# Kernel optimization log

Hardware: AMD Instinct MI355X
Metric: run time of the kernel (lower is better)

Reference implementation:

```python
import jax, jax.numpy as jnp
import numpy as np

NEG = jnp.float32(-9e15)
SLOPE = 0.2  # LeakyReLU negative slope used in LocalAggregator


def setup_inputs() -> dict:
    key = jax.random.key(0)
    k1, k2, k3, k4, k5, k6, k7 = jax.random.split(key, 7)
    B, N, D, V = 32, 200, 100, 50000
    stdv = 1.0 / np.sqrt(D)
    inputs = jax.random.randint(k1, (B, N), 0, V)
    adj = jax.random.randint(k2, (B, N, N), 0, 5).astype(jnp.int32)
    mask_item = jnp.ones((B, N), dtype=jnp.int32)
    emb = jax.random.uniform(k3, (V, D), jnp.float32, -stdv, stdv)
    a0 = jax.random.uniform(k4, (D, 1), jnp.float32, -stdv, stdv)
    a1 = jax.random.uniform(k5, (D, 1), jnp.float32, -stdv, stdv)
    a2 = jax.random.uniform(k6, (D, 1), jnp.float32, -stdv, stdv)
    a3 = jax.random.uniform(k7, (D, 1), jnp.float32, -stdv, stdv)
    return {"inputs": inputs, "adj": adj, "mask_item": mask_item,
            "emb": emb, "a0": a0, "a1": a1, "a2": a2, "a3": a3}


def reference(inputs, adj, mask_item, emb, a0, a1, a2, a3):
    # h: [B, N, D] session item embeddings
    h = emb[inputs]
    # e_k[b,i,j] = leaky_relu(sum_d h[b,i,d]*h[b,j,d]*a_k[d])
    # (equivalent to the original (h_i * h_j) @ a_k without the BxNxNxD blowup)
    def edge_score(a):
        s = jnp.einsum('bid,bjd->bij', h * a[:, 0][None, None, :], h)
        return jax.nn.leaky_relu(s, SLOPE)
    e0, e1, e2, e3 = edge_score(a0), edge_score(a1), edge_score(a2), edge_score(a3)
    alpha = jnp.where(adj == 1, e0, NEG)
    alpha = jnp.where(adj == 2, e1, alpha)
    alpha = jnp.where(adj == 3, e2, alpha)
    alpha = jnp.where(adj == 4, e3, alpha)
    alpha = jax.nn.softmax(alpha, axis=-1)  # [B, N, N]
    # weighted aggregation over neighbors; dropout_local is inactive in eval
    return jnp.einsum('bij,bjd->bid', alpha, h)
```

## Files before the change

kernel.cpp:

```cpp
#include <hip/hip_runtime.h>
#include <math.h>

#define NEGV  (-9e15f)
#define SLOPE 0.2f

typedef __fp16 f16;
typedef __fp16 f16x4 __attribute__((ext_vector_type(4)));
typedef __fp16 f16x8 __attribute__((ext_vector_type(8)));
typedef float  f32x4 __attribute__((ext_vector_type(4)));

__global__ __launch_bounds__(256) void gat_mfma_kernel(
    const int*   __restrict__ inputs,
    const int*   __restrict__ adj,
    const float* __restrict__ emb,
    const float* __restrict__ a0, const float* __restrict__ a1,
    const float* __restrict__ a2, const float* __restrict__ a3,
    float*       __restrict__ out)
{
    const int b   = blockIdx.x / 13;
    const int i0  = (blockIdx.x % 13) * 16;
    const int tid = threadIdx.x;

    __shared__ f16 HF[200][112];
    __shared__ __align__(16) unsigned char ubuf[4 * 16 * 96 * 2];
    __shared__ f16 GT[4][16][32];
    __shared__ int   sidx[200];
    __shared__ float redmax[16][4];
    __shared__ float redsum[16][4];

    f16 (*GF)[16][96] = (f16(*)[16][96])ubuf;
    f16 (*ST)[24]     = (f16(*)[24])ubuf;

    for (int t = tid; t < 200; t += 256) sidx[t] = inputs[b * 200 + t];
    __syncthreads();

    if (tid < 200) {
        const float4* src = (const float4*)(emb + (size_t)sidx[tid] * 100);
        f16x4* dst = (f16x4*)&HF[tid][0];
        #pragma unroll
        for (int c = 0; c < 25; ++c) {
            const float4 v = src[c];
            f16x4 o; o[0] = (f16)v.x; o[1] = (f16)v.y; o[2] = (f16)v.z; o[3] = (f16)v.w;
            dst[c] = o;
        }
        const f16x4 z = {(f16)0.f, (f16)0.f, (f16)0.f, (f16)0.f};
        dst[25] = z; dst[26] = z; dst[27] = z;
    }

    for (int t = tid; t < 4 * 16 * 24; t += 256) {
        const int kk = t / (16 * 24);
        const int rm = t % (16 * 24);
        const int il = rm / 24;
        const int c  = rm % 24;
        const float* ak = (kk == 0) ? a0 : (kk == 1) ? a1 : (kk == 2) ? a2 : a3;
        const int gi = i0 + il;
        f16x4 o = {(f16)0.f, (f16)0.f, (f16)0.f, (f16)0.f};
        if (gi < 200) {
            const float4 hv = ((const float4*)(emb + (size_t)sidx[gi] * 100))[c];
            const float4 av = ((const float4*)ak)[c];
            o[0] = (f16)(hv.x * av.x); o[1] = (f16)(hv.y * av.y);
            o[2] = (f16)(hv.z * av.z); o[3] = (f16)(hv.w * av.w);
        }
        ((f16x4*)&GF[kk][il][0])[c] = o;
    }

    for (int t = tid; t < 4 * 16 * 8; t += 256) {
        const int kk = t / (16 * 8);
        const int rm = t % (16 * 8);
        const int il = rm / 8;
        const int c  = rm % 8;
        f16x4 o = {(f16)0.f, (f16)0.f, (f16)0.f, (f16)0.f};
        const int gi = i0 + il;
        if (c == 4 && gi < 200) {
            const float* ak = (kk == 0) ? a0 : (kk == 1) ? a1 : (kk == 2) ? a2 : a3;
            const float* hi = emb + (size_t)sidx[gi] * 100;
            o[0] = (f16)(hi[96] * ak[96]); o[1] = (f16)(hi[97] * ak[97]);
            o[2] = (f16)(hi[98] * ak[98]); o[3] = (f16)(hi[99] * ak[99]);
        }
        ((f16x4*)&GT[kk][il][0])[c] = o;
    }
    __syncthreads();

    const int wave = tid >> 6;
    const int lane = tid & 63;
    const int lj   = lane & 15;
    const int quad = lane >> 4;
    const int rbase = quad * 4;

    f32x4 acc[4][4];
    #pragma unroll
    for (int kk = 0; kk < 4; ++kk)
        #pragma unroll
        for (int jt = 0; jt < 4; ++jt)
            acc[kk][jt] = (f32x4){0.f, 0.f, 0.f, 0.f};

    #pragma unroll
    for (int jtidx = 0; jtidx < 4; ++jtidx) {
        const int j  = (wave + 4 * jtidx) * 16 + lj;
        const int jr = (j < 200) ? j : 0;
        const f16x8* Brow = (const f16x8*)&HF[jr][0];
        const f16x8 b0 = Brow[quad];
        const f16x8 b1 = Brow[4 + quad];
        const f16x8 b2 = Brow[8 + quad];
        const f16x8 b3 = Brow[10 + quad];
        #pragma unroll
        for (int kk = 0; kk < 4; ++kk) {
            const f16x8* Arow = (const f16x8*)&GF[kk][lj][0];
            f32x4 c = acc[kk][jtidx];
            c = __builtin_amdgcn_mfma_f32_16x16x32_f16(Arow[quad],     b0, c, 0, 0, 0);
            c = __builtin_amdgcn_mfma_f32_16x16x32_f16(Arow[4 + quad], b1, c, 0, 0, 0);
            c = __builtin_amdgcn_mfma_f32_16x16x32_f16(Arow[8 + quad], b2, c, 0, 0, 0);
            c = __builtin_amdgcn_mfma_f32_16x16x32_f16(((const f16x8*)&GT[kk][lj][0])[quad], b3, c, 0, 0, 0);
            acc[kk][jtidx] = c;
        }
    }

    float sel[4][4];
    #pragma unroll
    for (int jtidx = 0; jtidx < 4; ++jtidx) {
        const int j = (wave + 4 * jtidx) * 16 + lj;
        #pragma unroll
        for (int reg = 0; reg < 4; ++reg) {
            const int gi = i0 + rbase + reg;
            float s = NEGV;
            if (j < 200 && gi < 200) {
                const int k = adj[(size_t)(b * 200 + gi) * 200 + j];
                if (k >= 1 && k <= 4) {
                    const float v = (k == 1) ? acc[0][jtidx][reg]
                                  : (k == 2) ? acc[1][jtidx][reg]
                                  : (k == 3) ? acc[2][jtidx][reg]
                                  :            acc[3][jtidx][reg];
                    s = (v >= 0.f) ? v : SLOPE * v;
                }
            }
            sel[jtidx][reg] = s;
        }
    }

    #pragma unroll
    for (int reg = 0; reg < 4; ++reg) {
        float m = fmaxf(fmaxf(sel[0][reg], sel[1][reg]), fmaxf(sel[2][reg], sel[3][reg]));
        #pragma unroll
        for (int off = 1; off <= 8; off <<= 1) m = fmaxf(m, __shfl_xor(m, off, 16));
        if (lj == 0) redmax[rbase + reg][wave] = m;
    }
    __syncthreads();
    float m4[4], lsum[4];
    #pragma unroll
    for (int reg = 0; reg < 4; ++reg) {
        const float* rr = redmax[rbase + reg];
        m4[reg] = fmaxf(fmaxf(rr[0], rr[1]), fmaxf(rr[2], rr[3]));
        lsum[reg] = 0.f;
    }
    float e[4][4];
    #pragma unroll
    for (int jtidx = 0; jtidx < 4; ++jtidx)
        #pragma unroll
        for (int reg = 0; reg < 4; ++reg) {
            e[jtidx][reg] = __expf(sel[jtidx][reg] - m4[reg]);
            lsum[reg] += e[jtidx][reg];
        }
    #pragma unroll
    for (int reg = 0; reg < 4; ++reg) {
        float s = lsum[reg];
        #pragma unroll
        for (int off = 1; off <= 8; off <<= 1) s += __shfl_xor(s, off, 16);
        if (lj == 0) redsum[rbase + reg][wave] = s;
    }
    __syncthreads();
    float inv[4];
    #pragma unroll
    for (int reg = 0; reg < 4; ++reg) {
        const float* rr = redsum[rbase + reg];
        inv[reg] = 1.0f / (rr[0] + rr[1] + rr[2] + rr[3]);
    }
    #pragma unroll
    for (int jtidx = 0; jtidx < 4; ++jtidx) {
        const int j = (wave + 4 * jtidx) * 16 + lj;
        if (j < 200) {
            #pragma unroll
            for (int reg = 0; reg < 4; ++reg)
                ST[j][rbase + reg] = (f16)(e[jtidx][reg] * inv[reg]);
        }
    }
    __syncthreads();

    const int ig = tid & 7;
    const int dq = tid >> 3;
    f32x4 o[16];
    #pragma unroll
    for (int i = 0; i < 16; ++i) o[i] = (f32x4){0.f, 0.f, 0.f, 0.f};
    if (dq < 25) {
        for (int jj = 0; jj < 25; ++jj) {
            const int j = ig * 25 + jj;
            const f16x8 w0 = *(const f16x8*)&ST[j][0];
            const f16x8 w1 = *(const f16x8*)&ST[j][8];
            const f16x4 hv = *(const f16x4*)&HF[j][dq * 4];
            const float h0 = (float)hv[0], h1 = (float)hv[1],
                        h2 = (float)hv[2], h3 = (float)hv[3];
            #pragma unroll
            for (int i = 0; i < 8; ++i) {
                const float w = (float)w0[i];
                o[i][0] += w * h0; o[i][1] += w * h1; o[i][2] += w * h2; o[i][3] += w * h3;
            }
            #pragma unroll
            for (int i = 0; i < 8; ++i) {
                const float w = (float)w1[i];
                o[8 + i][0] += w * h0; o[8 + i][1] += w * h1; o[8 + i][2] += w * h2; o[8 + i][3] += w * h3;
            }
        }
    }
    #pragma unroll
    for (int i = 0; i < 16; ++i)
        #pragma unroll
        for (int c = 0; c < 4; ++c)
            #pragma unroll
            for (int off = 1; off <= 4; off <<= 1)
                o[i][c] += __shfl_xor(o[i][c], off, 8);
    if (ig == 0 && dq < 25) {
        #pragma unroll
        for (int i = 0; i < 16; ++i) {
            const int gi = i0 + i;
            if (gi < 200)
                ((f32x4*)out)[(size_t)(b * 200 + gi) * 25 + dq] = o[i];
        }
    }
}

extern "C" void kernel_launch(void* const* d_in, const int* in_sizes, int n_in,
                              void* d_out, int out_size, void* d_ws, size_t ws_size,
                              hipStream_t stream) {
    const int*   inputs = (const int*)  d_in[0];
    const int*   adj    = (const int*)  d_in[1];
    const float* emb    = (const float*)d_in[3];
    const float* a0     = (const float*)d_in[4];
    const float* a1     = (const float*)d_in[5];
    const float* a2     = (const float*)d_in[6];
    const float* a3     = (const float*)d_in[7];
    float*       out    = (float*)d_out;

    gat_mfma_kernel<<<dim3(32 * 13), dim3(256), 0, stream>>>(inputs, adj, emb, a0, a1, a2, a3, out);
}
```

Before: 106.1 us.

## Drop shared-memory HF staging; read neighbor embeddings directly from global memory

Removes the per-block fp16 copy of all 200 session embeddings into LDS. The MFMA B operands and the aggregation loop now read embeddings straight from global memory, converting to fp16 only where needed. The aggregation step keeps weights and embeddings in fp32. The A-operand staging is merged into one padded 128-wide buffer, removing the separate tail buffer. This trades LDS footprint and fill time for more global/L2 traffic, with repeated scattered gathers of the same rows across the 13 blocks per batch.

```diff
diff --git a/kernel.cpp b/kernel.cpp
--- a/kernel.cpp
+++ b/kernel.cpp
@@ -9,7 +9,7 @@
 typedef __fp16 f16x8 __attribute__((ext_vector_type(8)));
 typedef float  f32x4 __attribute__((ext_vector_type(4)));
 
-__global__ __launch_bounds__(256) void gat_mfma_kernel(
+__global__ __launch_bounds__(256) void gat_v9_kernel(
     const int*   __restrict__ inputs,
     const int*   __restrict__ adj,
     const float* __restrict__ emb,
@@ -21,70 +21,38 @@
     const int i0  = (blockIdx.x % 13) * 16;
     const int tid = threadIdx.x;
 
-    __shared__ f16 HF[200][112];
-    __shared__ __align__(16) unsigned char ubuf[4 * 16 * 96 * 2];
-    __shared__ f16 GT[4][16][32];
+    __shared__ f16   GF[4][16][136];
+    __shared__ float ST[200][20];
     __shared__ int   sidx[200];
-    __shared__ float redmax[16][4];
-    __shared__ float redsum[16][4];
-
-    f16 (*GF)[16][96] = (f16(*)[16][96])ubuf;
-    f16 (*ST)[24]     = (f16(*)[24])ubuf;
+    __shared__ float redm[16][4];
+    __shared__ float reds[16][4];
 
     for (int t = tid; t < 200; t += 256) sidx[t] = inputs[b * 200 + t];
     __syncthreads();
 
-    if (tid < 200) {
-        const float4* src = (const float4*)(emb + (size_t)sidx[tid] * 100);
-        f16x4* dst = (f16x4*)&HF[tid][0];
-        #pragma unroll
-        for (int c = 0; c < 25; ++c) {
-            const float4 v = src[c];
-            f16x4 o; o[0] = (f16)v.x; o[1] = (f16)v.y; o[2] = (f16)v.z; o[3] = (f16)v.w;
-            dst[c] = o;
-        }
-        const f16x4 z = {(f16)0.f, (f16)0.f, (f16)0.f, (f16)0.f};
-        dst[25] = z; dst[26] = z; dst[27] = z;
-    }
-
-    for (int t = tid; t < 4 * 16 * 24; t += 256) {
-        const int kk = t / (16 * 24);
-        const int rm = t % (16 * 24);
-        const int il = rm / 24;
-        const int c  = rm % 24;
-        const float* ak = (kk == 0) ? a0 : (kk == 1) ? a1 : (kk == 2) ? a2 : a3;
+    const float* aks[4] = {a0, a1, a2, a3};
+
+    for (int t = tid; t < 4 * 16 * 34; t += 256) {
+        const int kk = t / (16 * 34);
+        const int rm = t % (16 * 34);
+        const int il = rm / 34;
+        const int c  = rm % 34;
         const int gi = i0 + il;
         f16x4 o = {(f16)0.f, (f16)0.f, (f16)0.f, (f16)0.f};
-        if (gi < 200) {
+        if (gi < 200 && c < 25) {
             const float4 hv = ((const float4*)(emb + (size_t)sidx[gi] * 100))[c];
-            const float4 av = ((const float4*)ak)[c];
+            const float4 av = ((const float4*)aks[kk])[c];
             o[0] = (f16)(hv.x * av.x); o[1] = (f16)(hv.y * av.y);
             o[2] = (f16)(hv.z * av.z); o[3] = (f16)(hv.w * av.w);
         }
         ((f16x4*)&GF[kk][il][0])[c] = o;
     }
-
-    for (int t = tid; t < 4 * 16 * 8; t += 256) {
-        const int kk = t / (16 * 8);
-        const int rm = t % (16 * 8);
-        const int il = rm / 8;
-        const int c  = rm % 8;
-        f16x4 o = {(f16)0.f, (f16)0.f, (f16)0.f, (f16)0.f};
-        const int gi = i0 + il;
-        if (c == 4 && gi < 200) {
-            const float* ak = (kk == 0) ? a0 : (kk == 1) ? a1 : (kk == 2) ? a2 : a3;
-            const float* hi = emb + (size_t)sidx[gi] * 100;
-            o[0] = (f16)(hi[96] * ak[96]); o[1] = (f16)(hi[97] * ak[97]);
-            o[2] = (f16)(hi[98] * ak[98]); o[3] = (f16)(hi[99] * ak[99]);
-        }
-        ((f16x4*)&GT[kk][il][0])[c] = o;
-    }
-    __syncthreads();
-
-    const int wave = tid >> 6;
-    const int lane = tid & 63;
-    const int lj   = lane & 15;
-    const int quad = lane >> 4;
+    __syncthreads();
+
+    const int wave  = tid >> 6;
+    const int lane  = tid & 63;
+    const int lj    = lane & 15;
+    const int quad  = lane >> 4;
     const int rbase = quad * 4;
 
     f32x4 acc[4][4];
@@ -95,30 +63,43 @@
             acc[kk][jt] = (f32x4){0.f, 0.f, 0.f, 0.f};
 
     #pragma unroll
-    for (int jtidx = 0; jtidx < 4; ++jtidx) {
-        const int j  = (wave + 4 * jtidx) * 16 + lj;
-        const int jr = (j < 200) ? j : 0;
-        const f16x8* Brow = (const f16x8*)&HF[jr][0];
-        const f16x8 b0 = Brow[quad];
-        const f16x8 b1 = Brow[4 + quad];
-        const f16x8 b2 = Brow[8 + quad];
-        const f16x8 b3 = Brow[10 + quad];
+    for (int jt = 0; jt < 4; ++jt) {
+        const int j   = (wave + 4 * jt) * 16 + lj;
+        const int row = sidx[(j < 200) ? j : 199];
+        const float* hp = emb + (size_t)row * 100;
+        f16x8 bfr[4];
+        #pragma unroll
+        for (int ks = 0; ks < 4; ++ks) {
+            const int base = ks * 32 + quad * 8;
+            f16x8 bf = {(f16)0.f,(f16)0.f,(f16)0.f,(f16)0.f,
+                        (f16)0.f,(f16)0.f,(f16)0.f,(f16)0.f};
+            if (base <= 88) {
+                const float4 x = *(const float4*)(hp + base);
+                const float4 y = *(const float4*)(hp + base + 4);
+                bf[0]=(f16)x.x; bf[1]=(f16)x.y; bf[2]=(f16)x.z; bf[3]=(f16)x.w;
+                bf[4]=(f16)y.x; bf[5]=(f16)y.y; bf[6]=(f16)y.z; bf[7]=(f16)y.w;
+            } else if (base == 96) {
+                const float4 x = *(const float4*)(hp + 96);
+                bf[0]=(f16)x.x; bf[1]=(f16)x.y; bf[2]=(f16)x.z; bf[3]=(f16)x.w;
+            }
+            bfr[ks] = bf;
+        }
         #pragma unroll
         for (int kk = 0; kk < 4; ++kk) {
-            const f16x8* Arow = (const f16x8*)&GF[kk][lj][0];
-            f32x4 c = acc[kk][jtidx];
-            c = __builtin_amdgcn_mfma_f32_16x16x32_f16(Arow[quad],     b0, c, 0, 0, 0);
-            c = __builtin_amdgcn_mfma_f32_16x16x32_f16(Arow[4 + quad], b1, c, 0, 0, 0);
-            c = __builtin_amdgcn_mfma_f32_16x16x32_f16(Arow[8 + quad], b2, c, 0, 0, 0);
-            c = __builtin_amdgcn_mfma_f32_16x16x32_f16(((const f16x8*)&GT[kk][lj][0])[quad], b3, c, 0, 0, 0);
-            acc[kk][jtidx] = c;
+            const f16* gr = &GF[kk][lj][0];
+            f32x4 c = acc[kk][jt];
+            c = __builtin_amdgcn_mfma_f32_16x16x32_f16(*(const f16x8*)(gr +      quad * 8), bfr[0], c, 0, 0, 0);
+            c = __builtin_amdgcn_mfma_f32_16x16x32_f16(*(const f16x8*)(gr + 32 + quad * 8), bfr[1], c, 0, 0, 0);
+            c = __builtin_amdgcn_mfma_f32_16x16x32_f16(*(const f16x8*)(gr + 64 + quad * 8), bfr[2], c, 0, 0, 0);
+            c = __builtin_amdgcn_mfma_f32_16x16x32_f16(*(const f16x8*)(gr + 96 + quad * 8), bfr[3], c, 0, 0, 0);
+            acc[kk][jt] = c;
         }
     }
 
     float sel[4][4];
     #pragma unroll
-    for (int jtidx = 0; jtidx < 4; ++jtidx) {
-        const int j = (wave + 4 * jtidx) * 16 + lj;
+    for (int jt = 0; jt < 4; ++jt) {
+        const int j = (wave + 4 * jt) * 16 + lj;
         #pragma unroll
         for (int reg = 0; reg < 4; ++reg) {
             const int gi = i0 + rbase + reg;
@@ -126,14 +107,14 @@
             if (j < 200 && gi < 200) {
                 const int k = adj[(size_t)(b * 200 + gi) * 200 + j];
                 if (k >= 1 && k <= 4) {
-                    const float v = (k == 1) ? acc[0][jtidx][reg]
-                                  : (k == 2) ? acc[1][jtidx][reg]
-                                  : (k == 3) ? acc[2][jtidx][reg]
-                                  :            acc[3][jtidx][reg];
+                    const float v = (k == 1) ? acc[0][jt][reg]
+                                  : (k == 2) ? acc[1][jt][reg]
+                                  : (k == 3) ? acc[2][jt][reg]
+                                  :            acc[3][jt][reg];
                     s = (v >= 0.f) ? v : SLOPE * v;
                 }
             }
-            sel[jtidx][reg] = s;
+            sel[jt][reg] = s;
         }
     }
 
@@ -142,45 +123,45 @@
         float m = fmaxf(fmaxf(sel[0][reg], sel[1][reg]), fmaxf(sel[2][reg], sel[3][reg]));
         #pragma unroll
         for (int off = 1; off <= 8; off <<= 1) m = fmaxf(m, __shfl_xor(m, off, 16));
-        if (lj == 0) redmax[rbase + reg][wave] = m;
+        if (lj == 0) redm[rbase + reg][wave] = m;
     }
     __syncthreads();
     float m4[4], lsum[4];
     #pragma unroll
     for (int reg = 0; reg < 4; ++reg) {
-        const float* rr = redmax[rbase + reg];
+        const float* rr = redm[rbase + reg];
         m4[reg] = fmaxf(fmaxf(rr[0], rr[1]), fmaxf(rr[2], rr[3]));
         lsum[reg] = 0.f;
     }
     float e[4][4];
     #pragma unroll
-    for (int jtidx = 0; jtidx < 4; ++jtidx)
+    for (int jt = 0; jt < 4; ++jt)
         #pragma unroll
         for (int reg = 0; reg < 4; ++reg) {
-            e[jtidx][reg] = __expf(sel[jtidx][reg] - m4[reg]);
-            lsum[reg] += e[jtidx][reg];
+            e[jt][reg] = __expf(sel[jt][reg] - m4[reg]);
+            lsum[reg] += e[jt][reg];
         }
     #pragma unroll
     for (int reg = 0; reg < 4; ++reg) {
         float s = lsum[reg];
         #pragma unroll
         for (int off = 1; off <= 8; off <<= 1) s += __shfl_xor(s, off, 16);
-        if (lj == 0) redsum[rbase + reg][wave] = s;
+        if (lj == 0) reds[rbase + reg][wave] = s;
     }
     __syncthreads();
     float inv[4];
     #pragma unroll
     for (int reg = 0; reg < 4; ++reg) {
-        const float* rr = redsum[rbase + reg];
+        const float* rr = reds[rbase + reg];
         inv[reg] = 1.0f / (rr[0] + rr[1] + rr[2] + rr[3]);
     }
     #pragma unroll
-    for (int jtidx = 0; jtidx < 4; ++jtidx) {
-        const int j = (wave + 4 * jtidx) * 16 + lj;
+    for (int jt = 0; jt < 4; ++jt) {
+        const int j = (wave + 4 * jt) * 16 + lj;
         if (j < 200) {
             #pragma unroll
             for (int reg = 0; reg < 4; ++reg)
-                ST[j][rbase + reg] = (f16)(e[jtidx][reg] * inv[reg]);
+                ST[j][rbase + reg] = e[jt][reg] * inv[reg];
         }
     }
     __syncthreads();
@@ -193,20 +174,15 @@
     if (dq < 25) {
         for (int jj = 0; jj < 25; ++jj) {
             const int j = ig * 25 + jj;
-            const f16x8 w0 = *(const f16x8*)&ST[j][0];
-            const f16x8 w1 = *(const f16x8*)&ST[j][8];
-            const f16x4 hv = *(const f16x4*)&HF[j][dq * 4];
-            const float h0 = (float)hv[0], h1 = (float)hv[1],
-                        h2 = (float)hv[2], h3 = (float)hv[3];
-            #pragma unroll
-            for (int i = 0; i < 8; ++i) {
-                const float w = (float)w0[i];
-                o[i][0] += w * h0; o[i][1] += w * h1; o[i][2] += w * h2; o[i][3] += w * h3;
-            }
-            #pragma unroll
-            for (int i = 0; i < 8; ++i) {
-                const float w = (float)w1[i];
-                o[8 + i][0] += w * h0; o[8 + i][1] += w * h1; o[8 + i][2] += w * h2; o[8 + i][3] += w * h3;
+            f32x4 w4[4];
+            #pragma unroll
+            for (int c = 0; c < 4; ++c) w4[c] = ((const f32x4*)&ST[j][0])[c];
+            const float* w = (const float*)w4;
+            const float4 hv = ((const float4*)(emb + (size_t)sidx[j] * 100))[dq];
+            #pragma unroll
+            for (int i = 0; i < 16; ++i) {
+                o[i][0] += w[i] * hv.x; o[i][1] += w[i] * hv.y;
+                o[i][2] += w[i] * hv.z; o[i][3] += w[i] * hv.w;
             }
         }
     }
@@ -239,5 +215,5 @@
     const float* a3     = (const float*)d_in[7];
     float*       out    = (float*)d_out;
 
-    gat_mfma_kernel<<<dim3(32 * 13), dim3(256), 0, stream>>>(inputs, adj, emb, a0, a1, a2, a3, out);
+    gat_v9_kernel<<<dim3(32 * 13), dim3(256), 0, stream>>>(inputs, adj, emb, a0, a1, a2, a3, out);
 }
```

After: 111.2 us. 4.8% more time.
